# Kernel tuning notes

Hardware: AMD Instinct MI355X
Metric: run time of the kernel (lower is better)

## Reference

```python
import jax, jax.numpy as jnp
import numpy as np

B, S, D = 1, 2048, 2048
H, G, HD = 32, 8, 64
EPS = 1e-6
ROPE_BASE = 10000.0


def rms_norm(x, g):
    # torch RMSNorm computed in fp32 then cast back (PytorchRMSNorm wrapper)
    xf = x.astype(jnp.float32)
    y = xf * jax.lax.rsqrt(jnp.mean(xf * xf, axis=-1, keepdims=True) + EPS) * g.astype(jnp.float32)
    return y.astype(x.dtype)


def rotate_half(x):
    x1, x2 = jnp.split(x, 2, axis=-1)
    return jnp.concatenate([-x2, x1], axis=-1)


def apply_rope(x, cos, sin):
    # x: (b, h, s, hd); cos/sin: (s, hd)
    return x * cos[None, None] + rotate_half(x) * sin[None, None]


def setup_inputs() -> dict:
    key = jax.random.key(0)
    ks = jax.random.split(key, 8)
    x = jax.random.normal(ks[0], (B, S, D), dtype=jnp.float32)
    wq = jax.random.normal(ks[1], (H * HD, D), dtype=jnp.float32) * (D ** -0.5)
    wk = jax.random.normal(ks[2], (G * HD, D), dtype=jnp.float32) * (D ** -0.5)
    wv = jax.random.normal(ks[3], (G * HD, D), dtype=jnp.float32) * (D ** -0.5)
    wo = jax.random.normal(ks[4], (D, H * HD), dtype=jnp.float32) * (D ** -0.5)
    qg = jnp.ones((HD,), dtype=jnp.float32)
    kg = jnp.ones((HD,), dtype=jnp.float32)
    # RoPE tables (HF-style: duplicated half-dim frequencies)
    inv_freq = 1.0 / (ROPE_BASE ** (jnp.arange(0, HD, 2, dtype=jnp.float32) / HD))
    ang = jnp.arange(S, dtype=jnp.float32)[:, None] * inv_freq[None, :]  # (S, HD/2)
    emb = jnp.concatenate([ang, ang], axis=-1)  # (S, HD)
    cos = jnp.cos(emb)
    sin = jnp.sin(emb)
    # causal mask: True = future (upper-right triangle)
    mask = jnp.triu(jnp.ones((S, S), dtype=bool), k=1)
    return {"x": x, "mask": mask, "cos": cos, "sin": sin,
            "wq": wq, "wk": wk, "wv": wv, "wo": wo, "qg": qg, "kg": kg}


def reference(x, mask, cos, sin, wq, wk, wv, wo, qg, kg):
    b, s, _ = x.shape
    rep = H // G
    q = (x @ wq.T).reshape(b, s, H, HD).transpose(0, 2, 1, 3)   # (b,H,s,hd)
    k = (x @ wk.T).reshape(b, s, G, HD).transpose(0, 2, 1, 3)   # (b,G,s,hd)
    v = (x @ wv.T).reshape(b, s, G, HD).transpose(0, 2, 1, 3)
    q = rms_norm(q, qg)
    k = rms_norm(k, kg)
    q = apply_rope(q, cos[:s], sin[:s])
    k = apply_rope(k, cos[:s], sin[:s])
    k = jnp.repeat(k, rep, axis=1)  # (b,H,s,hd) GQA expansion
    v = jnp.repeat(v, rep, axis=1)
    scores = jnp.einsum('bhqd,bhkd->bhqk', q, k) * (HD ** -0.5)
    neg = jnp.finfo(scores.dtype).min / 2
    scores = jnp.where(mask[None, None, :s, :s], neg, scores)
    w = jax.nn.softmax(scores, axis=-1)
    ctx = jnp.einsum('bhqk,bhkd->bhqd', w, v)
    ctx = ctx.transpose(0, 2, 1, 3).reshape(b, s, H * HD)
    return ctx @ wo.T
```

## Files before the change

### kernel.cpp

```cpp
#include <hip/hip_runtime.h>
#include <stdint.h>

#define SEQ    2048
#define DMODEL 2048
#define NHEAD  32
#define NKV    8
#define HDIM   64
#define NQKV   3072

typedef __bf16 bf16x8 __attribute__((ext_vector_type(8)));
typedef float  f32x4  __attribute__((ext_vector_type(4)));

#define SCALE2 0.180336880f
#define THR2   12.0f

__device__ __forceinline__ ushort bf(float f){
  __bf16 h = (__bf16)f;
  return __builtin_bit_cast(unsigned short, h);
}
__device__ __forceinline__ float b2f(ushort v){
  union { uint32_t u; float f; } a; a.u = ((uint32_t)v) << 16; return a.f;
}

__device__ __forceinline__ void gl_lds16(const void* g, void* l){
  __builtin_amdgcn_global_load_lds(
      (const __attribute__((address_space(1))) uint32_t*)g,
      (__attribute__((address_space(3))) uint32_t*)l, 16, 0, 0);
}

__global__ __launch_bounds__(256) void k_cvt_all(const float* __restrict__ x,
                                                 const float* __restrict__ wq,
                                                 const float* __restrict__ wk,
                                                 const float* __restrict__ wv,
                                                 const float* __restrict__ wo,
                                                 ushort* __restrict__ xb,
                                                 ushort* __restrict__ wcat,
                                                 ushort* __restrict__ wob){
  int i = blockIdx.x * 256 + threadIdx.x;
  const float* src; ushort* dst; int s4; int d4;
  if (i < 1048576)      { src = x;  dst = xb;   s4 = i;           d4 = s4; }
  else if (i < 2097152) { src = wq; dst = wcat; s4 = i - 1048576; d4 = s4; }
  else if (i < 2359296) { src = wk; dst = wcat; s4 = i - 2097152; d4 = s4 + 1048576; }
  else if (i < 2621440) { src = wv; dst = wcat; s4 = i - 2359296; d4 = s4 + 1310720; }
  else                  { src = wo; dst = wob;  s4 = i - 2621440; d4 = s4; }
  float4 v = reinterpret_cast<const float4*>(src)[s4];
  ushort4 o;
  o.x = bf(v.x); o.y = bf(v.y); o.z = bf(v.z); o.w = bf(v.w);
  reinterpret_cast<ushort4*>(dst)[d4] = o;
}

__global__ __launch_bounds__(256) void k_gemm_bt(const ushort* __restrict__ A,
                                                 const ushort* __restrict__ B,
                                                 float* __restrict__ C,
                                                 int M, int N, int K){
  __shared__ ushort As[2][128*64];
  __shared__ ushort Bs[2][128*64];
  const int tid = threadIdx.x, lane = tid & 63, wid = tid >> 6;
  const int bm = blockIdx.y * 128, bn = blockIdx.x * 128;
  const int wr = wid >> 1, wc = wid & 1;
  const int l15 = lane & 15, u = lane >> 4;

  const int srow = wid*32 + (lane >> 3);
  const int scol = ((lane & 7) ^ (lane >> 3)) * 8;
  const ushort* Abase = A + (size_t)(bm + srow) * K + scol;
  const ushort* Bbase = B + (size_t)(bn + srow) * K + scol;

  auto STAGE = [&](int buf, int k0){
#pragma unroll
    for (int c = 0; c < 4; c++){
      gl_lds16(Abase + k0 + (size_t)c*8*K, &As[buf][(wid*32 + c*8)*64]);
      gl_lds16(Bbase + k0 + (size_t)c*8*K, &Bs[buf][(wid*32 + c*8)*64]);
    }
  };

  f32x4 acc[4][4] = {};
  const int NT = K >> 6;

  STAGE(0, 0);
  __syncthreads();

  for (int t = 0; t < NT; t++){
    const int cur = t & 1;
    if (t + 1 < NT) STAGE(cur ^ 1, (t + 1) << 6);

#pragma unroll
    for (int kc = 0; kc < 2; kc++){
      bf16x8 af[4], bfr[4];
#pragma unroll
      for (int m = 0; m < 4; m++){
        int row = wr*64 + m*16 + l15;
        af[m] = *reinterpret_cast<const bf16x8*>(&As[cur][row*64 + (((kc*4+u) ^ (row&7))*8)]);
      }
#pragma unroll
      for (int n = 0; n < 4; n++){
        int row = wc*64 + n*16 + l15;
        bfr[n] = *reinterpret_cast<const bf16x8*>(&Bs[cur][row*64 + (((kc*4+u) ^ (row&7))*8)]);
      }
      __builtin_amdgcn_s_setprio(1);
#pragma unroll
      for (int m = 0; m < 4; m++)
#pragma unroll
        for (int n = 0; n < 4; n++)
          acc[m][n] = __builtin_amdgcn_mfma_f32_16x16x32_bf16(af[m], bfr[n], acc[m][n], 0, 0, 0);
      __builtin_amdgcn_s_setprio(0);
    }

    __syncthreads();
  }

#pragma unroll
  for (int m = 0; m < 4; m++)
#pragma unroll
    for (int n = 0; n < 4; n++)
#pragma unroll
      for (int j = 0; j < 4; j++){
        int row = bm + wr*64 + m*16 + u*4 + j;
        int col = bn + wc*64 + n*16 + l15;
        C[(size_t)row * N + col] = acc[m][n][j];
      }
}

__global__ __launch_bounds__(256) void k_gemm_btc(const ushort* __restrict__ A,
                                                  const ushort* __restrict__ B,
                                                  ushort* __restrict__ C,
                                                  int M, int N, int K){
  __shared__ ushort As[2][128*64];
  __shared__ ushort Bs[2][128*64];
  const int tid = threadIdx.x, lane = tid & 63, wid = tid >> 6;
  const int bm = blockIdx.y * 128, bn = blockIdx.x * 128;
  const int wr = wid >> 1, wc = wid & 1;
  const int l15 = lane & 15, u = lane >> 4;

  const int srow = wid*32 + (lane >> 3);
  const int scol = ((lane & 7) ^ (lane >> 3)) * 8;
  const ushort* Abase = A + (size_t)(bm + srow) * K + scol;
  const ushort* Bbase = B + (size_t)(bn + srow) * K + scol;

  auto STAGE = [&](int buf, int k0){
#pragma unroll
    for (int c = 0; c < 4; c++){
      gl_lds16(Abase + k0 + (size_t)c*8*K, &As[buf][(wid*32 + c*8)*64]);
      gl_lds16(Bbase + k0 + (size_t)c*8*K, &Bs[buf][(wid*32 + c*8)*64]);
    }
  };

  f32x4 acc[4][4] = {};
  const int NT = K >> 6;

  STAGE(0, 0);
  __syncthreads();

  for (int t = 0; t < NT; t++){
    const int cur = t & 1;
    if (t + 1 < NT) STAGE(cur ^ 1, (t + 1) << 6);

#pragma unroll
    for (int kc = 0; kc < 2; kc++){
      bf16x8 af[4], bfr[4];
#pragma unroll
      for (int m = 0; m < 4; m++){
        int row = wr*64 + m*16 + l15;
        af[m] = *reinterpret_cast<const bf16x8*>(&As[cur][row*64 + (((kc*4+u) ^ (row&7))*8)]);
      }
#pragma unroll
      for (int n = 0; n < 4; n++){
        int row = wc*64 + n*16 + l15;
        bfr[n] = *reinterpret_cast<const bf16x8*>(&Bs[cur][row*64 + (((kc*4+u) ^ (row&7))*8)]);
      }
      __builtin_amdgcn_s_setprio(1);
#pragma unroll
      for (int m = 0; m < 4; m++)
#pragma unroll
        for (int n = 0; n < 4; n++)
          acc[m][n] = __builtin_amdgcn_mfma_f32_16x16x32_bf16(af[m], bfr[n], acc[m][n], 0, 0, 0);
      __builtin_amdgcn_s_setprio(0);
    }

    __syncthreads();
  }

#pragma unroll
  for (int m = 0; m < 4; m++)
#pragma unroll
    for (int n = 0; n < 4; n++)
#pragma unroll
      for (int j = 0; j < 4; j++){
        int row = bm + wr*64 + m*16 + u*4 + j;
        int col = bn + wc*64 + n*16 + l15;
        C[(size_t)row * N + col] = bf(acc[m][n][j]);
      }
}

__global__ __launch_bounds__(256) void k_normrope(const ushort* __restrict__ qkvc,
                                                  const float* __restrict__ cosp,
                                                  const float* __restrict__ sinp,
                                                  const float* __restrict__ qg,
                                                  const float* __restrict__ kg,
                                                  ushort* __restrict__ qb,
                                                  ushort* __restrict__ kb){
  const int s = blockIdx.x;
  const int tid = threadIdx.x, lane = tid & 63, wid = tid >> 6;
  const ushort* row = qkvc + (size_t)s * NQKV;
  const float cs = cosp[s*HDIM + lane];
  const float sn = sinp[s*HDIM + lane];

  for (int hidx = wid; hidx < 40; hidx += 4){
    const bool isq = hidx < 32;
    const int col = isq ? hidx*64 : 2048 + (hidx-32)*64;
    float x = b2f(row[col + lane]);
    float ss = x * x;
#pragma unroll
    for (int m = 1; m < 64; m <<= 1) ss += __shfl_xor(ss, m);
    float r = rsqrtf(ss * (1.0f/64.0f) + 1e-6f);
    float y = x * r * (isq ? qg : kg)[lane];
    float p = __shfl_xor(y, 32);
    float out = y * cs + (lane < 32 ? -p : p) * sn;
    if (isq) qb[(size_t)s*2048 + hidx*64 + lane] = bf(out * SCALE2);
    else     kb[(size_t)s*512 + (hidx-32)*64 + lane] = bf(out);
  }
}

__global__ __launch_bounds__(256) void k_vtrans(const ushort* __restrict__ qkvc,
                                                ushort* __restrict__ vtb){
  __shared__ ushort tile[64][68];
  const int g = blockIdx.x >> 5, st = blockIdx.x & 31;
  const int tid = threadIdx.x;
#pragma unroll
  for (int i = 0; i < 4; i++){
    int idx = i*256 + tid;
    int r = idx >> 4, c4 = idx & 15;
    ushort4 v = *reinterpret_cast<const ushort4*>(
        qkvc + (size_t)(st*64 + r)*NQKV + 2560 + g*64 + c4*4);
    tile[c4*4+0][r] = v.x;
    tile[c4*4+1][r] = v.y;
    tile[c4*4+2][r] = v.z;
    tile[c4*4+3][r] = v.w;
  }
  __syncthreads();
#pragma unroll
  for (int i = 0; i < 4; i++){
    int idx = i*256 + tid;
    int d = idx >> 4, s4 = idx & 15;
    int pos4 = (s4 >> 3)*32 + (s4 & 3)*8 + ((s4 >> 2) & 1)*4;
    ushort4 o = *reinterpret_cast<const ushort4*>(&tile[d][s4*4]);
    *reinterpret_cast<ushort4*>(vtb + (size_t)(g*64 + d)*SEQ + st*64 + pos4) = o;
  }
}

__global__ __launch_bounds__(256) void k_attn(const ushort* __restrict__ qbuf,
                                              const ushort* __restrict__ kbuf,
                                              const ushort* __restrict__ vtb,
                                              ushort* __restrict__ ctx){
  __shared__ ushort Kd[2][64*64];
  __shared__ ushort Vd[2][64*64];

  const int bx = blockIdx.x;
  const int c  = bx & 255, sl = bx >> 8;
  const int cg = c >> 5,  h  = c & 31;
  const int qt = (sl == 0) ? 31 - cg : (sl == 1) ? 16 + cg
               : (sl == 2) ? 15 - cg : cg;
  const int g = h >> 2;
  const int tid = threadIdx.x, lane = tid & 63, wid = tid >> 6;
  const int l15 = lane & 15, u = lane >> 4;
  const int q0 = qt*64 + wid*16;
  const int tmax = qt;

  bf16x8 qf[2];
#pragma unroll
  for (int kc = 0; kc < 2; kc++)
    qf[kc] = *reinterpret_cast<const bf16x8*>(
        qbuf + (size_t)(q0 + l15)*2048 + h*64 + kc*32 + u*8);

  f32x4 o[4] = {};
  float mrun = -1e30f;
  float lrun = 0.f;

  int koff[8], voff[8];
#pragma unroll
  for (int kb = 0; kb < 4; kb++)
#pragma unroll
    for (int kc = 0; kc < 2; kc++){
      int keyl = kb*16 + l15;
      koff[kb*2+kc] = (keyl*64 + (((kc*4+u) ^ (keyl&7))*8)) * 2;
    }
#pragma unroll
  for (int kc = 0; kc < 2; kc++)
#pragma unroll
    for (int d0 = 0; d0 < 4; d0++){
      int vrow = d0*16 + l15;
      voff[kc*4+d0] = (vrow*64 + (((kc*4+u) ^ (vrow&7))*8)) * 2;
    }

  const int srow = wid*16 + (lane >> 3);
  const int scol = ((lane & 7) ^ (lane >> 3)) * 8;
  const ushort* ksrc0 = kbuf + (size_t)srow*512 + g*64 + scol;
  const ushort* vsrc0 = vtb  + (size_t)(g*64 + srow)*SEQ + scol;

  auto STAGE = [&](int buf, int t){
    const ushort* ks = ksrc0 + (size_t)t*64*512;
    gl_lds16(ks,         &Kd[buf][wid*1024]);
    gl_lds16(ks + 8*512, &Kd[buf][wid*1024 + 512]);
    const ushort* vs = vsrc0 + t*64;
    gl_lds16(vs,          &Vd[buf][wid*1024]);
    gl_lds16(vs + 8*SEQ,  &Vd[buf][wid*1024 + 512]);
  };

  STAGE(0, 0);
  __syncthreads();

  for (int t = 0; t <= tmax; t++){
    const int cur = t & 1;
    if (t < tmax) STAGE(cur ^ 1, t + 1);

    const char* KB = (const char*)Kd + cur*8192;
    const char* VB = (const char*)Vd + cur*8192;
    const bool full = (t*64 + 63) <= q0;

    f32x4 st[4];
#pragma unroll
    for (int kb = 0; kb < 4; kb++){
      const int key0 = t*64 + kb*16;
      if (key0 <= q0 + 15){
        bf16x8 kf0 = *reinterpret_cast<const bf16x8*>(KB + koff[kb*2]);
        bf16x8 kf1 = *reinterpret_cast<const bf16x8*>(KB + koff[kb*2+1]);
        f32x4 a = {};
        a = __builtin_amdgcn_mfma_f32_16x16x32_bf16(kf0, qf[0], a, 0, 0, 0);
        a = __builtin_amdgcn_mfma_f32_16x16x32_bf16(kf1, qf[1], a, 0, 0, 0);
        st[kb] = a;
      } else {
        st[kb] = (f32x4){-1e30f, -1e30f, -1e30f, -1e30f};
      }
    }
    if (!full){
      const int keyb = t*64 + u*4;
      const int qr = q0 + l15;
#pragma unroll
      for (int kb = 0; kb < 4; kb++)
#pragma unroll
        for (int j = 0; j < 4; j++)
          st[kb][j] = (keyb + kb*16 + j > qr) ? -1e30f : st[kb][j];
    }

    {
      f32x4 mx = st[0];
#pragma unroll
      for (int kb = 1; kb < 4; kb++)
#pragma unroll
        for (int j = 0; j < 4; j++) mx[j] = fmaxf(mx[j], st[kb][j]);
      float tml = fmaxf(fmaxf(mx[0], mx[1]), fmaxf(mx[2], mx[3]));
      if (__any(tml > mrun + THR2)){
        float tm = fmaxf(tml, __shfl_xor(tml, 16));
        tm = fmaxf(tm, __shfl_xor(tm, 32));
        float mn = fmaxf(mrun, tm);
        float al = exp2f(mrun - mn);
        mrun = mn;
        lrun *= al;
#pragma unroll
        for (int d0 = 0; d0 < 4; d0++)
#pragma unroll
          for (int j = 0; j < 4; j++) o[d0][j] *= al;
      }
#pragma unroll
      for (int kb = 0; kb < 4; kb++)
#pragma unroll
        for (int j = 0; j < 4; j++){
          float p = exp2f(st[kb][j] - mrun);
          st[kb][j] = p;
          lrun += p;
        }
    }

    __builtin_amdgcn_s_setprio(1);
#pragma unroll
    for (int kc = 0; kc < 2; kc++){
      union { uint32_t w[4]; bf16x8 v; } pb;
      asm("v_cvt_pk_bf16_f32 %0, %1, %2" : "=v"(pb.w[0]) : "v"(st[2*kc  ][0]), "v"(st[2*kc  ][1]));
      asm("v_cvt_pk_bf16_f32 %0, %1, %2" : "=v"(pb.w[1]) : "v"(st[2*kc  ][2]), "v"(st[2*kc  ][3]));
      asm("v_cvt_pk_bf16_f32 %0, %1, %2" : "=v"(pb.w[2]) : "v"(st[2*kc+1][0]), "v"(st[2*kc+1][1]));
      asm("v_cvt_pk_bf16_f32 %0, %1, %2" : "=v"(pb.w[3]) : "v"(st[2*kc+1][2]), "v"(st[2*kc+1][3]));
#pragma unroll
      for (int d0 = 0; d0 < 4; d0++){
        bf16x8 vb8 = *reinterpret_cast<const bf16x8*>(VB + voff[kc*4+d0]);
        o[d0] = __builtin_amdgcn_mfma_f32_16x16x32_bf16(vb8, pb.v, o[d0], 0, 0, 0);
      }
    }
    __builtin_amdgcn_s_setprio(0);

    __syncthreads();
  }

  {
    float lt = lrun + __shfl_xor(lrun, 16);
    lt += __shfl_xor(lt, 32);
    float inv = 1.0f / lt;
#pragma unroll
    for (int d0 = 0; d0 < 4; d0++){
      ushort4 w;
      w.x = bf(o[d0][0] * inv); w.y = bf(o[d0][1] * inv);
      w.z = bf(o[d0][2] * inv); w.w = bf(o[d0][3] * inv);
      *reinterpret_cast<ushort4*>(
          &ctx[(size_t)(q0 + l15)*2048 + h*64 + d0*16 + u*4]) = w;
    }
  }
}

extern "C" void kernel_launch(void* const* d_in, const int* in_sizes, int n_in,
                              void* d_out, int out_size, void* d_ws, size_t ws_size,
                              hipStream_t stream){
  const float* x    = (const float*)d_in[0];
  const float* cosp = (const float*)d_in[2];
  const float* sinp = (const float*)d_in[3];
  const float* wq   = (const float*)d_in[4];
  const float* wk   = (const float*)d_in[5];
  const float* wv   = (const float*)d_in[6];
  const float* wo   = (const float*)d_in[7];
  const float* qg   = (const float*)d_in[8];
  const float* kg   = (const float*)d_in[9];
  float* out = (float*)d_out;

  char* ws = (char*)d_ws;
  ushort* xb   = (ushort*)(ws);
  ushort* wcat = (ushort*)(ws + 8388608);
  ushort* wob  = (ushort*)(ws + 20971520);
  ushort* qkvc = (ushort*)(ws + 29360128);
  ushort* qb   = (ushort*)(ws + 41943040);
  ushort* kb   = (ushort*)(ws + 50331648);
  ushort* vtb  = (ushort*)(ws + 52428800);
  ushort* ctxb = (ushort*)(ws + 54525952);

  k_cvt_all<<<14336, 256, 0, stream>>>(x, wq, wk, wv, wo, xb, wcat, wob);
  k_gemm_btc<<<dim3(24, 16), 256, 0, stream>>>(xb, wcat, qkvc, 2048, 3072, 2048);
  k_normrope<<<2048, 256, 0, stream>>>(qkvc, cosp, sinp, qg, kg, qb, kb);
  k_vtrans<<<256, 256, 0, stream>>>(qkvc, vtb);
  k_attn<<<1024, 256, 0, stream>>>(qb, kb, vtb, ctxb);
  k_gemm_bt<<<dim3(16, 16), 256, 0, stream>>>(ctxb, wob, out, 2048, 2048, 2048);
}
```

Measured before the change: 150.5 us.

## Split causal attention KV range into two partitions with a combine kernel

Each query-tile/head pair in the attention kernel now processes only half of its causal key range. The grid doubles and the old interleaved tile ordering is replaced by a simple descending schedule. Each partition writes an unnormalized-then-normalized bf16 partial output plus its running max and sum. A new combine kernel merges the two partials with log-sum-exp weights into the context buffer. This aims to increase parallelism and shorten the longest per-block loops, at the cost of an extra launch, extra global traffic for the partials, and an added bf16 rounding of the intermediate.

```diff
diff --git a/kernel.cpp b/kernel.cpp
--- a/kernel.cpp
+++ b/kernel.cpp
@@ -250,20 +250,23 @@
 __global__ __launch_bounds__(256) void k_attn(const ushort* __restrict__ qbuf,
                                               const ushort* __restrict__ kbuf,
                                               const ushort* __restrict__ vtb,
-                                              ushort* __restrict__ ctx){
+                                              ushort* __restrict__ op,
+                                              float2* __restrict__ ml){
   __shared__ ushort Kd[2][64*64];
   __shared__ ushort Vd[2][64*64];
 
   const int bx = blockIdx.x;
-  const int c  = bx & 255, sl = bx >> 8;
-  const int cg = c >> 5,  h  = c & 31;
-  const int qt = (sl == 0) ? 31 - cg : (sl == 1) ? 16 + cg
-               : (sl == 2) ? 15 - cg : cg;
+  const int qt   = 31 - (bx >> 6);
+  const int part = (bx >> 5) & 1;
+  const int h    = bx & 31;
   const int g = h >> 2;
+  const int n  = qt + 1;
+  const int h1 = (n + 1) >> 1;
+  const int t0 = part ? h1 : 0;
+  const int t1 = part ? n  : h1;
   const int tid = threadIdx.x, lane = tid & 63, wid = tid >> 6;
   const int l15 = lane & 15, u = lane >> 4;
   const int q0 = qt*64 + wid*16;
-  const int tmax = qt;
 
   bf16x8 qf[2];
 #pragma unroll
@@ -305,102 +308,132 @@
     gl_lds16(vs + 8*SEQ,  &Vd[buf][wid*1024 + 512]);
   };
 
-  STAGE(0, 0);
-  __syncthreads();
-
-  for (int t = 0; t <= tmax; t++){
-    const int cur = t & 1;
-    if (t < tmax) STAGE(cur ^ 1, t + 1);
-
-    const char* KB = (const char*)Kd + cur*8192;
-    const char* VB = (const char*)Vd + cur*8192;
-    const bool full = (t*64 + 63) <= q0;
-
-    f32x4 st[4];
-#pragma unroll
-    for (int kb = 0; kb < 4; kb++){
-      const int key0 = t*64 + kb*16;
-      if (key0 <= q0 + 15){
-        bf16x8 kf0 = *reinterpret_cast<const bf16x8*>(KB + koff[kb*2]);
-        bf16x8 kf1 = *reinterpret_cast<const bf16x8*>(KB + koff[kb*2+1]);
-        f32x4 a = {};
-        a = __builtin_amdgcn_mfma_f32_16x16x32_bf16(kf0, qf[0], a, 0, 0, 0);
-        a = __builtin_amdgcn_mfma_f32_16x16x32_bf16(kf1, qf[1], a, 0, 0, 0);
-        st[kb] = a;
-      } else {
-        st[kb] = (f32x4){-1e30f, -1e30f, -1e30f, -1e30f};
-      }
-    }
-    if (!full){
-      const int keyb = t*64 + u*4;
-      const int qr = q0 + l15;
-#pragma unroll
-      for (int kb = 0; kb < 4; kb++)
-#pragma unroll
-        for (int j = 0; j < 4; j++)
-          st[kb][j] = (keyb + kb*16 + j > qr) ? -1e30f : st[kb][j];
-    }
-
-    {
-      f32x4 mx = st[0];
-#pragma unroll
-      for (int kb = 1; kb < 4; kb++)
-#pragma unroll
-        for (int j = 0; j < 4; j++) mx[j] = fmaxf(mx[j], st[kb][j]);
-      float tml = fmaxf(fmaxf(mx[0], mx[1]), fmaxf(mx[2], mx[3]));
-      if (__any(tml > mrun + THR2)){
-        float tm = fmaxf(tml, __shfl_xor(tml, 16));
-        tm = fmaxf(tm, __shfl_xor(tm, 32));
-        float mn = fmaxf(mrun, tm);
-        float al = exp2f(mrun - mn);
-        mrun = mn;
-        lrun *= al;
-#pragma unroll
-        for (int d0 = 0; d0 < 4; d0++)
-#pragma unroll
-          for (int j = 0; j < 4; j++) o[d0][j] *= al;
-      }
-#pragma unroll
-      for (int kb = 0; kb < 4; kb++)
-#pragma unroll
-        for (int j = 0; j < 4; j++){
-          float p = exp2f(st[kb][j] - mrun);
-          st[kb][j] = p;
-          lrun += p;
+  if (t0 < t1){
+    STAGE(0, t0);
+    __syncthreads();
+
+    for (int t = t0; t < t1; t++){
+      const int cur = (t - t0) & 1;
+      if (t + 1 < t1) STAGE(cur ^ 1, t + 1);
+
+      const char* KB = (const char*)Kd + cur*8192;
+      const char* VB = (const char*)Vd + cur*8192;
+      const bool full = (t*64 + 63) <= q0;
+
+      f32x4 st[4];
+#pragma unroll
+      for (int kb = 0; kb < 4; kb++){
+        const int key0 = t*64 + kb*16;
+        if (key0 <= q0 + 15){
+          bf16x8 kf0 = *reinterpret_cast<const bf16x8*>(KB + koff[kb*2]);
+          bf16x8 kf1 = *reinterpret_cast<const bf16x8*>(KB + koff[kb*2+1]);
+          f32x4 a = {};
+          a = __builtin_amdgcn_mfma_f32_16x16x32_bf16(kf0, qf[0], a, 0, 0, 0);
+          a = __builtin_amdgcn_mfma_f32_16x16x32_bf16(kf1, qf[1], a, 0, 0, 0);
+          st[kb] = a;
+        } else {
+          st[kb] = (f32x4){-1e30f, -1e30f, -1e30f, -1e30f};
         }
-    }
-
-    __builtin_amdgcn_s_setprio(1);
-#pragma unroll
-    for (int kc = 0; kc < 2; kc++){
-      union { uint32_t w[4]; bf16x8 v; } pb;
-      asm("v_cvt_pk_bf16_f32 %0, %1, %2" : "=v"(pb.w[0]) : "v"(st[2*kc  ][0]), "v"(st[2*kc  ][1]));
-      asm("v_cvt_pk_bf16_f32 %0, %1, %2" : "=v"(pb.w[1]) : "v"(st[2*kc  ][2]), "v"(st[2*kc  ][3]));
-      asm("v_cvt_pk_bf16_f32 %0, %1, %2" : "=v"(pb.w[2]) : "v"(st[2*kc+1][0]), "v"(st[2*kc+1][1]));
-      asm("v_cvt_pk_bf16_f32 %0, %1, %2" : "=v"(pb.w[3]) : "v"(st[2*kc+1][2]), "v"(st[2*kc+1][3]));
-#pragma unroll
-      for (int d0 = 0; d0 < 4; d0++){
-        bf16x8 vb8 = *reinterpret_cast<const bf16x8*>(VB + voff[kc*4+d0]);
-        o[d0] = __builtin_amdgcn_mfma_f32_16x16x32_bf16(vb8, pb.v, o[d0], 0, 0, 0);
-      }
-    }
-    __builtin_amdgcn_s_setprio(0);
-
-    __syncthreads();
+      }
+      if (!full){
+        const int keyb = t*64 + u*4;
+        const int qr = q0 + l15;
+#pragma unroll
+        for (int kb = 0; kb < 4; kb++)
+#pragma unroll
+          for (int j = 0; j < 4; j++)
+            st[kb][j] = (keyb + kb*16 + j > qr) ? -1e30f : st[kb][j];
+      }
+
+      {
+        f32x4 mx = st[0];
+#pragma unroll
+        for (int kb = 1; kb < 4; kb++)
+#pragma unroll
+          for (int j = 0; j < 4; j++) mx[j] = fmaxf(mx[j], st[kb][j]);
+        float tml = fmaxf(fmaxf(mx[0], mx[1]), fmaxf(mx[2], mx[3]));
+        if (__any(tml > mrun + THR2)){
+          float tm = fmaxf(tml, __shfl_xor(tml, 16));
+          tm = fmaxf(tm, __shfl_xor(tm, 32));
+          float mn = fmaxf(mrun, tm);
+          float al = exp2f(mrun - mn);
+          mrun = mn;
+          lrun *= al;
+#pragma unroll
+          for (int d0 = 0; d0 < 4; d0++)
+#pragma unroll
+            for (int j = 0; j < 4; j++) o[d0][j] *= al;
+        }
+#pragma unroll
+        for (int kb = 0; kb < 4; kb++)
+#pragma unroll
+          for (int j = 0; j < 4; j++){
+            float p = exp2f(st[kb][j] - mrun);
+            st[kb][j] = p;
+            lrun += p;
+          }
+      }
+
+      __builtin_amdgcn_s_setprio(1);
+#pragma unroll
+      for (int kc = 0; kc < 2; kc++){
+        union { uint32_t w[4]; bf16x8 v; } pb;
+        asm("v_cvt_pk_bf16_f32 %0, %1, %2" : "=v"(pb.w[0]) : "v"(st[2*kc  ][0]), "v"(st[2*kc  ][1]));
+        asm("v_cvt_pk_bf16_f32 %0, %1, %2" : "=v"(pb.w[1]) : "v"(st[2*kc  ][2]), "v"(st[2*kc  ][3]));
+        asm("v_cvt_pk_bf16_f32 %0, %1, %2" : "=v"(pb.w[2]) : "v"(st[2*kc+1][0]), "v"(st[2*kc+1][1]));
+        asm("v_cvt_pk_bf16_f32 %0, %1, %2" : "=v"(pb.w[3]) : "v"(st[2*kc+1][2]), "v"(st[2*kc+1][3]));
+#pragma unroll
+        for (int d0 = 0; d0 < 4; d0++){
+          bf16x8 vb8 = *reinterpret_cast<const bf16x8*>(VB + voff[kc*4+d0]);
+          o[d0] = __builtin_amdgcn_mfma_f32_16x16x32_bf16(vb8, pb.v, o[d0], 0, 0, 0);
+        }
+      }
+      __builtin_amdgcn_s_setprio(0);
+
+      __syncthreads();
+    }
   }
 
   {
     float lt = lrun + __shfl_xor(lrun, 16);
     lt += __shfl_xor(lt, 32);
-    float inv = 1.0f / lt;
+    float inv = lt > 0.f ? 1.0f / lt : 0.f;
+    const size_t ridx = (size_t)part*65536 + h*2048 + (q0 + l15);
 #pragma unroll
     for (int d0 = 0; d0 < 4; d0++){
       ushort4 w;
       w.x = bf(o[d0][0] * inv); w.y = bf(o[d0][1] * inv);
       w.z = bf(o[d0][2] * inv); w.w = bf(o[d0][3] * inv);
-      *reinterpret_cast<ushort4*>(
-          &ctx[(size_t)(q0 + l15)*2048 + h*64 + d0*16 + u*4]) = w;
-    }
+      *reinterpret_cast<ushort4*>(&op[ridx*64 + d0*16 + u*4]) = w;
+    }
+    if (lane < 16) ml[ridx] = make_float2(mrun, lt);
+  }
+}
+
+__global__ __launch_bounds__(256) void k_comb(const ushort* __restrict__ op,
+                                              const float2* __restrict__ ml,
+                                              ushort* __restrict__ ctx){
+  const int tq = blockIdx.x*256 + threadIdx.x;
+  const int q = tq & 3, row = (tq >> 2) & 2047, h = tq >> 13;
+  const int idx = h*2048 + row;
+  float2 a = ml[idx], b = ml[idx + 65536];
+  float m = fmaxf(a.x, b.x);
+  float w0 = exp2f(a.x - m) * a.y;
+  float w1 = exp2f(b.x - m) * b.y;
+  float inv = 1.0f / (w0 + w1);
+  w0 *= inv; w1 *= inv;
+  const ushort4* p0 = reinterpret_cast<const ushort4*>(op + (size_t)idx*64 + q*16);
+  const ushort4* p1 = reinterpret_cast<const ushort4*>(op + ((size_t)idx + 65536)*64 + q*16);
+  ushort* dst = ctx + (size_t)row*2048 + h*64 + q*16;
+#pragma unroll
+  for (int i = 0; i < 4; i++){
+    ushort4 x0 = p0[i], x1 = p1[i];
+    ushort4 w;
+    w.x = bf(w0*b2f(x0.x) + w1*b2f(x1.x));
+    w.y = bf(w0*b2f(x0.y) + w1*b2f(x1.y));
+    w.z = bf(w0*b2f(x0.z) + w1*b2f(x1.z));
+    w.w = bf(w0*b2f(x0.w) + w1*b2f(x1.w));
+    reinterpret_cast<ushort4*>(dst)[i] = w;
   }
 }
 
@@ -427,11 +460,14 @@
   ushort* kb   = (ushort*)(ws + 50331648);
   ushort* vtb  = (ushort*)(ws + 52428800);
   ushort* ctxb = (ushort*)(ws + 54525952);
+  ushort* op   = (ushort*)(ws);
+  float2* ml   = (float2*)(ws + 16777216);
 
   k_cvt_all<<<14336, 256, 0, stream>>>(x, wq, wk, wv, wo, xb, wcat, wob);
   k_gemm_btc<<<dim3(24, 16), 256, 0, stream>>>(xb, wcat, qkvc, 2048, 3072, 2048);
   k_normrope<<<2048, 256, 0, stream>>>(qkvc, cosp, sinp, qg, kg, qb, kb);
   k_vtrans<<<256, 256, 0, stream>>>(qkvc, vtb);
-  k_attn<<<1024, 256, 0, stream>>>(qb, kb, vtb, ctxb);
+  k_attn<<<2048, 256, 0, stream>>>(qb, kb, vtb, op, ml);
+  k_comb<<<1024, 256, 0, stream>>>(op, ml, ctxb);
   k_gemm_bt<<<dim3(16, 16), 256, 0, stream>>>(ctxb, wob, out, 2048, 2048, 2048);
 }
```

Result: no change. 148.6 us (-1.2%).
